# Optimization experiments

Measured on AMD Instinct MI355X. Metric: run time of the kernel, lower is better.

The kernel has to match this reference:

```python
import jax, jax.numpy as jnp
import numpy as np
from jax import lax

G = 8  # number of RBF grid points (FastKAN default style)
GRID = jnp.linspace(-2.0, 2.0, G)
DENOM = 4.0 / (G - 1)  # grid spacing used as gaussian width


def _fastkan_conv(x, ln_w, ln_b, Wb, bb, Ws):
    # x: [B, C, H, W]; 3x3 conv, stride 1, pad 1 via patch unfold + FastKAN linear
    B, C, H, W = x.shape
    p = lax.conv_general_dilated_patches(x, (3, 3), (1, 1), ((1, 1), (1, 1)))  # [B, C*9, H, W]
    p = p.transpose(0, 2, 3, 1).reshape(B * H * W, C * 9)  # [N, in]
    # LayerNorm over patch features (FastKAN normalizes before the RBF basis)
    mu = p.mean(-1, keepdims=True)
    var = p.var(-1, keepdims=True)
    pn = (p - mu) / jnp.sqrt(var + 1e-5) * ln_w + ln_b
    # Gaussian RBF basis: [N, in, G]
    rbf = jnp.exp(-jnp.square((pn[:, :, None] - GRID) / DENOM))
    spline = rbf.reshape(B * H * W, -1) @ Ws.T          # [N, out]
    base = jax.nn.silu(p) @ Wb.T + bb                    # [N, out]
    out = spline + base
    return out.reshape(B, H, W, -1).transpose(0, 3, 1, 2)  # [B, out, H, W]


def _bn_relu_pool(h, gamma, beta):
    # BatchNorm2d in training mode (batch stats), ReLU, MaxPool2d(2,2)
    mu = h.mean((0, 2, 3), keepdims=True)
    var = h.var((0, 2, 3), keepdims=True)
    h = (h - mu) / jnp.sqrt(var + 1e-5) * gamma[None, :, None, None] + beta[None, :, None, None]
    h = jax.nn.relu(h)
    return lax.reduce_window(h, -jnp.inf, lax.max, (1, 1, 2, 2), (1, 1, 2, 2), 'VALID')


def setup_inputs() -> dict:
    key = jax.random.key(0)
    ks = jax.random.split(key, 16)
    B, Cin, H, W = 32, 16, 64, 64
    dims = [(Cin * 9, 64), (64 * 9, 128), (128 * 9, 256)]
    inp = {"x": jax.random.normal(ks[0], (B, Cin, H, W), jnp.float32)}
    for i, (fin, fout) in enumerate(dims, 1):
        inp[f"ln_w{i}"] = jnp.ones((fin,), jnp.float32)
        inp[f"ln_b{i}"] = jnp.zeros((fin,), jnp.float32)
        inp[f"Wb{i}"] = jax.random.normal(ks[3 * i], (fout, fin), jnp.float32) * 0.05
        inp[f"bb{i}"] = jnp.zeros((fout,), jnp.float32)
        inp[f"Ws{i}"] = jax.random.normal(ks[3 * i + 1], (fout, fin * G), jnp.float32) * 0.05
        inp[f"g{i}"] = jnp.ones((fout,), jnp.float32)
        inp[f"be{i}"] = jnp.zeros((fout,), jnp.float32)
    return inp


def reference(x, ln_w1, ln_b1, Wb1, bb1, Ws1, g1, be1,
              ln_w2, ln_b2, Wb2, bb2, Ws2, g2, be2,
              ln_w3, ln_b3, Wb3, bb3, Ws3, g3, be3):
    h = _bn_relu_pool(_fastkan_conv(x, ln_w1, ln_b1, Wb1, bb1, Ws1), g1, be1)
    h = _bn_relu_pool(_fastkan_conv(h, ln_w2, ln_b2, Wb2, bb2, Ws2), g2, be2)
    h = _bn_relu_pool(_fastkan_conv(h, ln_w3, ln_b3, Wb3, bb3, Ws3), g3, be3)
    return h.reshape(h.shape[0], -1)  # flatten: [B, 256*8*8]
```

## Files before the change

kernel.cpp:

```cpp
#include <hip/hip_runtime.h>

typedef _Float16 half_t;
typedef __attribute__((ext_vector_type(8))) _Float16 half8;
typedef __attribute__((ext_vector_type(4))) float floatx4;


#define RBF_SCALE 2.1019644f
#define RBF_G0   -4.2039288f
#define RBF_2D    2.40224482f
#define RBF_D2    1.44269504f
#define RBF_Q     0.13533528f

template<int C, int H, int W>
__global__ __launch_bounds__(256)
void ln_prep(const float* __restrict__ x,
             const float* __restrict__ lnw, const float* __restrict__ lnb,
             half_t* __restrict__ pn, half_t* __restrict__ sp)
{
    const int HW = H * W, IN = C * 9;
    const int NL = (IN + 63) / 64;
    __shared__ float xw[C * 57];

    const int wv = threadIdx.x >> 6, lane = threadIdx.x & 63;
    const int pix0 = blockIdx.x * 16;
    const int b = pix0 / HW, hw0 = pix0 % HW;
    const int h = hw0 / W, x0 = hw0 % W;
    const float* xb = x + (long)b * C * HW;

    for (int idx = threadIdx.x; idx < C * 54; idx += 256) {
        int ch = idx / 54, rem = idx - ch * 54;
        int dy = rem / 18, col = rem - dy * 18;
        int y = h + dy - 1, xx = x0 + col - 1;
        float v = 0.f;
        if (y >= 0 && y < H && xx >= 0 && xx < W)
            v = xb[(long)ch * HW + y * W + xx];
        xw[ch * 57 + dy * 19 + col] = v;
    }
    __syncthreads();

    int  ga[NL];
    float lw[NL], lb[NL];
    #pragma unroll
    for (int t = 0; t < NL; ++t) {
        int i = t * 64 + lane;
        if (i < IN) {
            int ch = i / 9, r = i - ch * 9;
            int dy = r / 3, dx = r - dy * 3;
            ga[t] = ch * 57 + dy * 19 + dx;
            lw[t] = lnw[i];
            lb[t] = lnb[i];
        } else { ga[t] = 0; lw[t] = 0.f; lb[t] = 0.f; }
    }

    #pragma unroll
    for (int p = 0; p < 4; ++p) {
        const int px = wv * 4 + p;
        const int pix = pix0 + px;

        float v[NL];
        float s = 0.f, s2 = 0.f;
        #pragma unroll
        for (int t = 0; t < NL; ++t) {
            int i = t * 64 + lane;
            float val = (i < IN) ? xw[ga[t] + px] : 0.f;
            v[t] = val; s += val; s2 += val * val;
        }
        #pragma unroll
        for (int off = 32; off > 0; off >>= 1) {
            s  += __shfl_down(s,  off, 64);
            s2 += __shfl_down(s2, off, 64);
        }
        s = __shfl(s, 0, 64); s2 = __shfl(s2, 0, 64);
        float mean = s / IN;
        float istd = rsqrtf(s2 / IN - mean * mean + 1e-5f);

        #pragma unroll
        for (int t = 0; t < NL; ++t) {
            int i = t * 64 + lane;
            if (i < IN) {
                float val = v[t];
                float pnv = (val - mean) * istd * lw[t] + lb[t];
                pnv = fminf(12.f, fmaxf(-12.f, pnv * RBF_SCALE));
                pn[(long)pix * IN + i] = (half_t)pnv;
                sp[(long)pix * IN + i] = (half_t)(val / (1.f + __expf(-val)));
            }
        }
    }
}

template<int IN, int OUT>
__global__ __launch_bounds__(256)
void conv_w(const float* __restrict__ Ws, const float* __restrict__ Wb,
            half_t* __restrict__ Wt)
{
    const int NIB = (IN + 63) / 64, NSTEP = NIB * 9;
    int idx = blockIdx.x * 256 + threadIdx.x;
    if (idx >= OUT * NSTEP * 64) return;
    int uu = idx & 63;
    int t = idx >> 6;
    int o = t % OUT;
    int s = t / OUT;
    int iblk = s / 9, j = s % 9;
    int ulin = (((uu >> 3) ^ (o & 7)) << 3) + (uu & 7);
    int i = iblk * 64 + ulin;
    float v = 0.f;
    if (i < IN)
        v = (j < 8) ? Ws[(long)o * IN * 8 + i * 8 + j] : Wb[(long)o * IN + i];
    Wt[idx] = (half_t)v;
}

template<int IN, int OUT, int HW, int NB, int SPLIT>
__global__ __launch_bounds__(256)
void kan_gemm(const half_t* __restrict__ pn, const half_t* __restrict__ sp,
              const half_t* __restrict__ Wt, float* __restrict__ out)
{
    const int NIB = (IN + 63) / 64;

    __shared__ half_t As[64 * 64];
    __shared__ half_t Bs[NB * 64 * 64];

    const int tid = threadIdx.x;
    const int row = tid >> 2, q = tid & 3;
    const int pix = blockIdx.x * 64 + row;
    const half_t* pnrow = pn + (long)pix * IN;
    const half_t* sprow = sp + (long)pix * IN;

    const int wv = tid >> 6, lane = tid & 63;
    const int lr = lane & 15, lq = lane >> 4;
    const int u0 = (2 * q) ^ (row & 7);
    const int u1 = (2 * q + 1) ^ (row & 7);
    const int yoff = blockIdx.y * (4 * NB * 16);

    floatx4 acc[NB][4] = {};
    float r[16], u[16];
    half8 pf0, pf1;

    const int grpA = (blockIdx.z * NIB) / SPLIT;
    const int grpB = ((blockIdx.z + 1) * NIB) / SPLIT;
    const int s0 = grpA * 9, s1 = grpB * 9;

    int jg = 0, ibg = grpA;

    auto ldglob = [&](const half_t* base, int ib, half8& a, half8& b) {
        int i0 = ib * 64 + q * 16;
        const half_t* pp = base + ((i0 < IN) ? i0 : 0);
        a = *(const half8*)pp;
        b = *(const half8*)(pp + 8);
    };

    auto stageB = [&](int it) {
        const half_t* wsrc = Wt + (long)it * OUT * 64
                              + (long)(yoff + wv * NB * 16) * 64;
        #pragma unroll
        for (int c = 0; c < NB * 2; ++c) {
            __builtin_amdgcn_global_load_lds(
                (const __attribute__((address_space(1))) void*)(wsrc + c * 512 + lane * 8),
                (__attribute__((address_space(3))) void*)(&Bs[wv * NB * 1024 + c * 512]),
                16, 0, 0);
        }
    };

    auto genA = [&]() {
        if (jg < 8) {
            if (jg == 0) {
                #pragma unroll
                for (int kk = 0; kk < 8; ++kk) {
                    float d0 = (float)pf0[kk] - RBF_G0;
                    float d1 = (float)pf1[kk] - RBF_G0;
                    r[kk]     = __builtin_amdgcn_exp2f(-(d0 * d0));
                    u[kk]     = __builtin_amdgcn_exp2f(fmaf(RBF_2D, d0, -RBF_D2));
                    r[kk + 8] = __builtin_amdgcn_exp2f(-(d1 * d1));
                    u[kk + 8] = __builtin_amdgcn_exp2f(fmaf(RBF_2D, d1, -RBF_D2));
                }
            }
            half8 a0, a1;
            #pragma unroll
            for (int kk = 0; kk < 8; ++kk) {
                a0[kk] = (half_t)r[kk];
                a1[kk] = (half_t)r[kk + 8];
            }
            *(half8*)&As[row * 64 + u0 * 8] = a0;
            *(half8*)&As[row * 64 + u1 * 8] = a1;
            if (jg < 7) {
                #pragma unroll
                for (int kk = 0; kk < 16; ++kk) { r[kk] *= u[kk]; u[kk] *= RBF_Q; }
            }
            if (jg == 7) ldglob(sprow, ibg, pf0, pf1);
        } else {
            *(half8*)&As[row * 64 + u0 * 8] = pf0;
            *(half8*)&As[row * 64 + u1 * 8] = pf1;
            ldglob(pnrow, ibg + 1, pf0, pf1);
        }
        if (++jg == 9) { jg = 0; ++ibg; }
    };

    auto domfma = [&]() {
        __builtin_amdgcn_s_setprio(1);
        #pragma unroll
        for (int ks = 0; ks < 2; ++ks) {
            half8 af[4], bf[NB];
            #pragma unroll
            for (int mf = 0; mf < 4; ++mf) {
                int rr = mf * 16 + lr;
                af[mf] = *(const half8*)&As[rr * 64 + (((ks * 4 + lq) ^ (rr & 7)) * 8)];
            }
            #pragma unroll
            for (int nb = 0; nb < NB; ++nb) {
                int rr = wv * NB * 16 + nb * 16 + lr;
                bf[nb] = *(const half8*)&Bs[rr * 64 + (((ks * 4 + lq) ^ (rr & 7)) * 8)];
            }
            #pragma unroll
            for (int nb = 0; nb < NB; ++nb)
                #pragma unroll
                for (int mf = 0; mf < 4; ++mf)
                    acc[nb][mf] = __builtin_amdgcn_mfma_f32_16x16x32_f16(
                        bf[nb], af[mf], acc[nb][mf], 0, 0, 0);
        }
        __builtin_amdgcn_s_setprio(0);
    };

    ldglob(pnrow, grpA, pf0, pf1);

    for (int it = s0; it < s1; ++it) {
        __syncthreads();
        stageB(it);
        genA();
        __syncthreads();
        domfma();
    }

    const long zoff = (long)blockIdx.z * ((long)gridDim.x * 64) * OUT;
    #pragma unroll
    for (int nb = 0; nb < NB; ++nb)
    #pragma unroll
    for (int mf = 0; mf < 4; ++mf)
    #pragma unroll
    for (int reg = 0; reg < 4; ++reg) {
        int o  = yoff + wv * NB * 16 + nb * 16 + lq * 4 + reg;
        int p2 = blockIdx.x * 64 + mf * 16 + lr;
        int b2 = p2 / HW, hw2 = p2 % HW;
        out[zoff + ((long)b2 * OUT + o) * HW + hw2] = acc[nb][mf][reg];
    }
}

__launch_bounds__(256)
__global__ void bn_stats(const float* __restrict__ h, const float* __restrict__ bias,
                         int C, int HW, int B, int nz, float* __restrict__ sums)
{
    int c = blockIdx.y;
    float bbc = bias[c];
    long zstride = (long)B * C * HW;
    int total = B * HW;
    float s = 0.f, s2 = 0.f;
    for (int idx = blockIdx.x * 256 + threadIdx.x; idx < total; idx += 256 * gridDim.x) {
        int b = idx / HW, r = idx % HW;
        long base = ((long)b * C + c) * HW + r;
        float v = bbc;
        for (int z = 0; z < nz; ++z) v += h[z * zstride + base];
        s += v; s2 += v * v;
    }
    for (int off = 32; off > 0; off >>= 1) {
        s  += __shfl_down(s,  off, 64);
        s2 += __shfl_down(s2, off, 64);
    }
    __shared__ float rs[4], rs2[4];
    int lane = threadIdx.x & 63, wid = threadIdx.x >> 6;
    if (lane == 0) { rs[wid] = s; rs2[wid] = s2; }
    __syncthreads();
    if (threadIdx.x == 0) {
        atomicAdd(&sums[c],     rs[0] + rs[1] + rs[2] + rs[3]);
        atomicAdd(&sums[C + c], rs2[0] + rs2[1] + rs2[2] + rs2[3]);
    }
}

__launch_bounds__(256)
__global__ void bn_relu_pool(const float* __restrict__ h, const float* __restrict__ sums,
                             const float* __restrict__ bias,
                             const float* __restrict__ gamma, const float* __restrict__ beta,
                             float* __restrict__ out, int B, int C, int H, int W, int nz)
{
    int Ho = H / 2, Wo = W / 2;
    long total = (long)B * C * Ho * Wo;
    long idx = (long)blockIdx.x * 256 + threadIdx.x;
    if (idx >= total) return;
    int pw = idx % Wo; long t = idx / Wo;
    int ph = t % Ho; t /= Ho;
    int c = t % C; int b = (int)(t / C);

    float M = (float)B * H * W;
    float mean = sums[c] / M;
    float var  = sums[C + c] / M - mean * mean;
    float scale = gamma[c] * rsqrtf(var + 1e-5f);
    float shift = beta[c] - mean * scale + bias[c] * scale;

    long zstride = (long)B * C * H * W;
    const float* hp = h + ((long)b * C + c) * H * W;
    float m = 0.f;
    #pragma unroll
    for (int i = 0; i < 2; ++i)
        #pragma unroll
        for (int j = 0; j < 2; ++j) {
            long off = (2 * ph + i) * W + 2 * pw + j;
            float v = 0.f;
            for (int z = 0; z < nz; ++z) v += hp[z * zstride + off];
            v = v * scale + shift;
            m = fmaxf(m, v);
        }
    out[idx] = m;
}

extern "C" void kernel_launch(void* const* d_in, const int* in_sizes, int n_in,
                              void* d_out, int out_size, void* d_ws, size_t ws_size,
                              hipStream_t stream) {
    const float* x     = (const float*)d_in[0];
    const float* ln_w1 = (const float*)d_in[1];  const float* ln_b1 = (const float*)d_in[2];
    const float* Wb1   = (const float*)d_in[3];  const float* bb1   = (const float*)d_in[4];
    const float* Ws1   = (const float*)d_in[5];  const float* g1    = (const float*)d_in[6];
    const float* be1   = (const float*)d_in[7];
    const float* ln_w2 = (const float*)d_in[8];  const float* ln_b2 = (const float*)d_in[9];
    const float* Wb2   = (const float*)d_in[10]; const float* bb2   = (const float*)d_in[11];
    const float* Ws2   = (const float*)d_in[12]; const float* g2    = (const float*)d_in[13];
    const float* be2   = (const float*)d_in[14];
    const float* ln_w3 = (const float*)d_in[15]; const float* ln_b3 = (const float*)d_in[16];
    const float* Wb3   = (const float*)d_in[17]; const float* bb3   = (const float*)d_in[18];
    const float* Ws3   = (const float*)d_in[19]; const float* g3    = (const float*)d_in[20];
    const float* be3   = (const float*)d_in[21];

    const int B = 32;
    char* ws = (char*)d_ws;
    float*  convbuf = (float*)(ws + 0);
    float*  poolbuf = (float*)(ws + 33554432);
    float*  stats1  = (float*)(ws + 41943040);
    float*  stats2  = (float*)(ws + 41945088);
    float*  stats3  = (float*)(ws + 41947136);
    half_t* wt1     = (half_t*)(ws + 41949184);
    half_t* wt2     = (half_t*)(ws + 42170368);
    half_t* wt3     = (half_t*)(ws + 43497472);
    half_t* pnbuf   = (half_t*)(ws + 48805888);
    half_t* spbuf   = (half_t*)(ws + 86554624);

    hipMemsetAsync(stats1, 0, 6144, stream);

    conv_w<144, 64><<<(64 * 27 * 64 + 255) / 256, 256, 0, stream>>>(Ws1, Wb1, wt1);
    conv_w<576, 128><<<(128 * 81 * 64 + 255) / 256, 256, 0, stream>>>(Ws2, Wb2, wt2);
    conv_w<1152, 256><<<(256 * 162 * 64 + 255) / 256, 256, 0, stream>>>(Ws3, Wb3, wt3);

    {
        const int H = 64, W = 64, OUT = 64;
        int npix = B * H * W;
        ln_prep<16, H, W><<<npix / 16, 256, 0, stream>>>(x, ln_w1, ln_b1, pnbuf, spbuf);
        kan_gemm<144, OUT, H * W, 1, 1><<<dim3(npix / 64, 1, 1), 256, 0, stream>>>(
            pnbuf, spbuf, wt1, convbuf);
        bn_stats<<<dim3(64, OUT), 256, 0, stream>>>(convbuf, bb1, OUT, H * W, B, 1, stats1);
        long tot = (long)B * OUT * (H / 2) * (W / 2);
        bn_relu_pool<<<(tot + 255) / 256, 256, 0, stream>>>(
            convbuf, stats1, bb1, g1, be1, poolbuf, B, OUT, H, W, 1);
    }
    {
        const int H = 32, W = 32, OUT = 128;
        int npix = B * H * W;
        ln_prep<64, H, W><<<npix / 16, 256, 0, stream>>>(poolbuf, ln_w2, ln_b2, pnbuf, spbuf);
        kan_gemm<576, OUT, H * W, 2, 2><<<dim3(npix / 64, 1, 2), 256, 0, stream>>>(
            pnbuf, spbuf, wt2, convbuf);
        bn_stats<<<dim3(16, OUT), 256, 0, stream>>>(convbuf, bb2, OUT, H * W, B, 2, stats2);
        long tot = (long)B * OUT * (H / 2) * (W / 2);
        bn_relu_pool<<<(tot + 255) / 256, 256, 0, stream>>>(
            convbuf, stats2, bb2, g2, be2, poolbuf, B, OUT, H, W, 2);
    }
    {
        const int H = 16, W = 16, OUT = 256;
        int npix = B * H * W;
        ln_prep<128, H, W><<<npix / 16, 256, 0, stream>>>(poolbuf, ln_w3, ln_b3, pnbuf, spbuf);
        kan_gemm<1152, OUT, H * W, 2, 4><<<dim3(npix / 64, 2, 4), 256, 0, stream>>>(
            pnbuf, spbuf, wt3, convbuf);
        bn_stats<<<dim3(8, OUT), 256, 0, stream>>>(convbuf, bb3, OUT, H * W, B, 4, stats3);
        long tot = (long)B * OUT * (H / 2) * (W / 2);
        bn_relu_pool<<<(tot + 255) / 256, 256, 0, stream>>>(
            convbuf, stats3, bb3, g3, be3, (float*)d_out, B, OUT, H, W, 4);
    }
}
```

Baseline: 465.6 us.

## Enlarge KAN GEMM tile to 128 pixels with 2x2 wave grid

Each block now covers 128 pixel rows instead of 64, and the four waves form a 2x2 grid over the M and N dimensions. Each thread generates RBF values for 32 elements instead of 16, which halves the number of blocks and raises reuse of each staged weight tile. The cost is more registers (r/u arrays grow to 32, more accumulators), fewer blocks for parallelism, and a larger A tile in shared memory.

```diff
diff --git a/kernel.cpp b/kernel.cpp
--- a/kernel.cpp
+++ b/kernel.cpp
@@ -109,31 +109,30 @@
     Wt[idx] = (half_t)v;
 }
 
-template<int IN, int OUT, int HW, int NB, int SPLIT>
+template<int IN, int OUT, int HW, int NF, int SPLIT>
 __global__ __launch_bounds__(256)
 void kan_gemm(const half_t* __restrict__ pn, const half_t* __restrict__ sp,
               const half_t* __restrict__ Wt, float* __restrict__ out)
 {
     const int NIB = (IN + 63) / 64;
 
-    __shared__ half_t As[64 * 64];
-    __shared__ half_t Bs[NB * 64 * 64];
+    __shared__ half_t As[128 * 64];
+    __shared__ half_t Bs[32 * NF * 64];
 
     const int tid = threadIdx.x;
-    const int row = tid >> 2, q = tid & 3;
-    const int pix = blockIdx.x * 64 + row;
-    const half_t* pnrow = pn + (long)pix * IN;
-    const half_t* sprow = sp + (long)pix * IN;
+    const int arow = tid >> 1, aq = tid & 1;
+    const int pix_a = blockIdx.x * 128 + arow;
+    const half_t* pnrow = pn + (long)pix_a * IN;
+    const half_t* sprow = sp + (long)pix_a * IN;
 
     const int wv = tid >> 6, lane = tid & 63;
     const int lr = lane & 15, lq = lane >> 4;
-    const int u0 = (2 * q) ^ (row & 7);
-    const int u1 = (2 * q + 1) ^ (row & 7);
-    const int yoff = blockIdx.y * (4 * NB * 16);
-
-    floatx4 acc[NB][4] = {};
-    float r[16], u[16];
-    half8 pf0, pf1;
+    const int wm = wv >> 1, wn = wv & 1;
+    const int yoff = blockIdx.y * (32 * NF);
+
+    floatx4 acc[NF][4] = {};
+    float r[32], u[32];
+    half8 pf[4];
 
     const int grpA = (blockIdx.z * NIB) / SPLIT;
     const int grpB = ((blockIdx.z + 1) * NIB) / SPLIT;
@@ -141,21 +140,23 @@
 
     int jg = 0, ibg = grpA;
 
-    auto ldglob = [&](const half_t* base, int ib, half8& a, half8& b) {
-        int i0 = ib * 64 + q * 16;
-        const half_t* pp = base + ((i0 < IN) ? i0 : 0);
-        a = *(const half8*)pp;
-        b = *(const half8*)(pp + 8);
+    auto ldglob = [&](const half_t* base, int ib) {
+        int i0 = ib * 64 + aq * 32;
+        #pragma unroll
+        for (int c = 0; c < 4; ++c) {
+            int ic = i0 + c * 8;
+            pf[c] = *(const half8*)(base + ((ic < IN) ? ic : 0));
+        }
     };
 
     auto stageB = [&](int it) {
-        const half_t* wsrc = Wt + (long)it * OUT * 64
-                              + (long)(yoff + wv * NB * 16) * 64;
-        #pragma unroll
-        for (int c = 0; c < NB * 2; ++c) {
+        const half_t* wsrc = Wt + ((long)it * OUT + yoff) * 64
+                              + wv * (NF * 512) + lane * 8;
+        #pragma unroll
+        for (int c = 0; c < NF; ++c) {
             __builtin_amdgcn_global_load_lds(
-                (const __attribute__((address_space(1))) void*)(wsrc + c * 512 + lane * 8),
-                (__attribute__((address_space(3))) void*)(&Bs[wv * NB * 1024 + c * 512]),
+                (const __attribute__((address_space(1))) void*)(wsrc + c * 512),
+                (__attribute__((address_space(3))) void*)(&Bs[wv * (NF * 512) + c * 512]),
                 16, 0, 0);
         }
     };
@@ -164,32 +165,31 @@
         if (jg < 8) {
             if (jg == 0) {
                 #pragma unroll
-                for (int kk = 0; kk < 8; ++kk) {
-                    float d0 = (float)pf0[kk] - RBF_G0;
-                    float d1 = (float)pf1[kk] - RBF_G0;
-                    r[kk]     = __builtin_amdgcn_exp2f(-(d0 * d0));
-                    u[kk]     = __builtin_amdgcn_exp2f(fmaf(RBF_2D, d0, -RBF_D2));
-                    r[kk + 8] = __builtin_amdgcn_exp2f(-(d1 * d1));
-                    u[kk + 8] = __builtin_amdgcn_exp2f(fmaf(RBF_2D, d1, -RBF_D2));
-                }
-            }
-            half8 a0, a1;
-            #pragma unroll
-            for (int kk = 0; kk < 8; ++kk) {
-                a0[kk] = (half_t)r[kk];
-                a1[kk] = (half_t)r[kk + 8];
-            }
-            *(half8*)&As[row * 64 + u0 * 8] = a0;
-            *(half8*)&As[row * 64 + u1 * 8] = a1;
+                for (int c = 0; c < 4; ++c)
+                    #pragma unroll
+                    for (int e = 0; e < 8; ++e) {
+                        float d = (float)pf[c][e] - RBF_G0;
+                        r[c * 8 + e] = __builtin_amdgcn_exp2f(-(d * d));
+                        u[c * 8 + e] = __builtin_amdgcn_exp2f(fmaf(RBF_2D, d, -RBF_D2));
+                    }
+            }
+            #pragma unroll
+            for (int c = 0; c < 4; ++c) {
+                half8 a;
+                #pragma unroll
+                for (int e = 0; e < 8; ++e) a[e] = (half_t)r[c * 8 + e];
+                *(half8*)&As[arow * 64 + (((aq * 4 + c) ^ (arow & 7)) * 8)] = a;
+            }
             if (jg < 7) {
                 #pragma unroll
-                for (int kk = 0; kk < 16; ++kk) { r[kk] *= u[kk]; u[kk] *= RBF_Q; }
-            }
-            if (jg == 7) ldglob(sprow, ibg, pf0, pf1);
+                for (int k = 0; k < 32; ++k) { r[k] *= u[k]; u[k] *= RBF_Q; }
+            }
+            if (jg == 7) ldglob(sprow, ibg);
         } else {
-            *(half8*)&As[row * 64 + u0 * 8] = pf0;
-            *(half8*)&As[row * 64 + u1 * 8] = pf1;
-            ldglob(pnrow, ibg + 1, pf0, pf1);
+            #pragma unroll
+            for (int c = 0; c < 4; ++c)
+                *(half8*)&As[arow * 64 + (((aq * 4 + c) ^ (arow & 7)) * 8)] = pf[c];
+            ldglob(pnrow, ibg + 1);
         }
         if (++jg == 9) { jg = 0; ++ibg; }
     };
@@ -198,19 +198,19 @@
         __builtin_amdgcn_s_setprio(1);
         #pragma unroll
         for (int ks = 0; ks < 2; ++ks) {
-            half8 af[4], bf[NB];
+            half8 af[4], bf[NF];
             #pragma unroll
             for (int mf = 0; mf < 4; ++mf) {
-                int rr = mf * 16 + lr;
-                af[mf] = *(const half8*)&As[rr * 64 + (((ks * 4 + lq) ^ (rr & 7)) * 8)];
-            }
-            #pragma unroll
-            for (int nb = 0; nb < NB; ++nb) {
-                int rr = wv * NB * 16 + nb * 16 + lr;
-                bf[nb] = *(const half8*)&Bs[rr * 64 + (((ks * 4 + lq) ^ (rr & 7)) * 8)];
-            }
-            #pragma unroll
-            for (int nb = 0; nb < NB; ++nb)
+                int r0 = wm * 64 + mf * 16 + lr;
+                af[mf] = *(const half8*)&As[r0 * 64 + (((ks * 4 + lq) ^ (r0 & 7)) * 8)];
+            }
+            #pragma unroll
+            for (int nb = 0; nb < NF; ++nb) {
+                int rb = wn * (16 * NF) + nb * 16 + lr;
+                bf[nb] = *(const half8*)&Bs[rb * 64 + (((ks * 4 + lq) ^ (rb & 7)) * 8)];
+            }
+            #pragma unroll
+            for (int nb = 0; nb < NF; ++nb)
                 #pragma unroll
                 for (int mf = 0; mf < 4; ++mf)
                     acc[nb][mf] = __builtin_amdgcn_mfma_f32_16x16x32_f16(
@@ -219,7 +219,7 @@
         __builtin_amdgcn_s_setprio(0);
     };
 
-    ldglob(pnrow, grpA, pf0, pf1);
+    ldglob(pnrow, grpA);
 
     for (int it = s0; it < s1; ++it) {
         __syncthreads();
@@ -229,15 +229,15 @@
         domfma();
     }
 
-    const long zoff = (long)blockIdx.z * ((long)gridDim.x * 64) * OUT;
-    #pragma unroll
-    for (int nb = 0; nb < NB; ++nb)
+    const long zoff = (long)blockIdx.z * ((long)gridDim.x * 128) * OUT;
+    #pragma unroll
+    for (int nb = 0; nb < NF; ++nb)
     #pragma unroll
     for (int mf = 0; mf < 4; ++mf)
     #pragma unroll
     for (int reg = 0; reg < 4; ++reg) {
-        int o  = yoff + wv * NB * 16 + nb * 16 + lq * 4 + reg;
-        int p2 = blockIdx.x * 64 + mf * 16 + lr;
+        int o  = yoff + wn * (16 * NF) + nb * 16 + lq * 4 + reg;
+        int p2 = blockIdx.x * 128 + wm * 64 + mf * 16 + lr;
         int b2 = p2 / HW, hw2 = p2 % HW;
         out[zoff + ((long)b2 * OUT + o) * HW + hw2] = acc[nb][mf][reg];
     }
@@ -349,7 +349,7 @@
         const int H = 64, W = 64, OUT = 64;
         int npix = B * H * W;
         ln_prep<16, H, W><<<npix / 16, 256, 0, stream>>>(x, ln_w1, ln_b1, pnbuf, spbuf);
-        kan_gemm<144, OUT, H * W, 1, 1><<<dim3(npix / 64, 1, 1), 256, 0, stream>>>(
+        kan_gemm<144, OUT, H * W, 2, 1><<<dim3(npix / 128, 1, 1), 256, 0, stream>>>(
             pnbuf, spbuf, wt1, convbuf);
         bn_stats<<<dim3(64, OUT), 256, 0, stream>>>(convbuf, bb1, OUT, H * W, B, 1, stats1);
         long tot = (long)B * OUT * (H / 2) * (W / 2);
@@ -360,7 +360,7 @@
         const int H = 32, W = 32, OUT = 128;
         int npix = B * H * W;
         ln_prep<64, H, W><<<npix / 16, 256, 0, stream>>>(poolbuf, ln_w2, ln_b2, pnbuf, spbuf);
-        kan_gemm<576, OUT, H * W, 2, 2><<<dim3(npix / 64, 1, 2), 256, 0, stream>>>(
+        kan_gemm<576, OUT, H * W, 4, 2><<<dim3(npix / 128, 1, 2), 256, 0, stream>>>(
             pnbuf, spbuf, wt2, convbuf);
         bn_stats<<<dim3(16, OUT), 256, 0, stream>>>(convbuf, bb2, OUT, H * W, B, 2, stats2);
         long tot = (long)B * OUT * (H / 2) * (W / 2);
@@ -371,7 +371,7 @@
         const int H = 16, W = 16, OUT = 256;
         int npix = B * H * W;
         ln_prep<128, H, W><<<npix / 16, 256, 0, stream>>>(poolbuf, ln_w3, ln_b3, pnbuf, spbuf);
-        kan_gemm<1152, OUT, H * W, 2, 4><<<dim3(npix / 64, 2, 4), 256, 0, stream>>>(
+        kan_gemm<1152, OUT, H * W, 4, 4><<<dim3(npix / 128, 2, 4), 256, 0, stream>>>(
             pnbuf, spbuf, wt3, convbuf);
         bn_stats<<<dim3(8, OUT), 256, 0, stream>>>(convbuf, bb3, OUT, H * W, B, 4, stats3);
         long tot = (long)B * OUT * (H / 2) * (W / 2);
```

Result: no change. 469.8 us (+0.9%).
